# Kernel optimization log

Hardware: AMD Instinct MI355X
Metric: run time of the kernel (lower is better)

Reference implementation:

```python
import jax, jax.numpy as jnp
import numpy as np
import math

IN_C = 1024
OUT_C = 1024
HEADS = 16
GROUPS = 4

def grouped_linear(src, weight, bias):
    # src: [..., in_c]; weight: [g, in_c//g, out_c//g]; bias: [out_c]
    g, icg, ocg = weight.shape
    lead = src.shape[:-1]
    s = src.reshape(*lead, g, icg)
    out = jnp.einsum('...gi,gio->...go', s, weight)
    out = out.reshape(*lead, g * ocg)
    return out + bias

def restricted_softmax(src, margin=0.0):
    src_max = jnp.maximum(jnp.max(src, axis=-1, keepdims=True), 0.0)
    out = jnp.exp(src - src_max)
    return out / (jnp.sum(out, axis=-1, keepdims=True) + jnp.exp(margin - src_max))

def setup_inputs() -> dict:
    key = jax.random.key(0)
    ks = jax.random.split(key, 9)
    B, S = 2, 2048
    icg, ocg = IN_C // GROUPS, OUT_C // GROUPS
    scale = 1.0 / math.sqrt(icg)
    return {
        'query': jax.random.normal(ks[0], (B, S, IN_C), jnp.float32),
        'key': jax.random.normal(ks[1], (B, S, IN_C), jnp.float32),
        'value': jax.random.normal(ks[2], (B, S, IN_C), jnp.float32),
        'wq': jax.random.uniform(ks[3], (GROUPS, icg, ocg), jnp.float32, -scale, scale),
        'wk': jax.random.uniform(ks[4], (GROUPS, icg, ocg), jnp.float32, -scale, scale),
        'wv': jax.random.uniform(ks[5], (GROUPS, icg, ocg), jnp.float32, -scale, scale),
        'bq': jax.random.uniform(ks[6], (OUT_C,), jnp.float32, -scale, scale),
        'bk': jax.random.uniform(ks[7], (OUT_C,), jnp.float32, -scale, scale),
        'bv': jax.random.uniform(ks[8], (OUT_C,), jnp.float32, -scale, scale),
    }

def reference(query, key, value, wq, wk, wv, bq, bk, bv):
    q = grouped_linear(query, wq, bq)   # [B,S,OUT_C]
    k = grouped_linear(key, wk, bk)
    v = grouped_linear(value, wv, bv)
    B, Sq, _ = q.shape
    Sk = k.shape[-2]
    d = OUT_C // HEADS
    q = q.reshape(B, Sq, HEADS, d).transpose(0, 2, 1, 3)  # [B,H,Sq,d]
    k = k.reshape(B, Sk, HEADS, d).transpose(0, 2, 1, 3)
    v = v.reshape(B, Sk, HEADS, d).transpose(0, 2, 1, 3)
    score = jnp.einsum('bhqd,bhkd->bhqk', q, k) / math.sqrt(d)
    attn = restricted_softmax(score)
    out = jnp.einsum('bhqk,bhkd->bhqd', attn, v)
    out = out.transpose(0, 2, 1, 3).reshape(B, Sq, OUT_C)
    return out
```

## Files before the change

kernel.cpp:

```cpp
#include <hip/hip_runtime.h>
#include <hip/hip_bf16.h>

#define BB 2
#define SS 2048
#define CC 1024
#define HH 16
#define DDIM 64
#define NROWS (BB*SS)

#define QSC 0.18033688011112042f

typedef __attribute__((ext_vector_type(8))) short bf16x8;
typedef __attribute__((ext_vector_type(4))) float f32x4;

__device__ __forceinline__ f32x4 mfma16(bf16x8 a, bf16x8 b, f32x4 c) {
    return __builtin_amdgcn_mfma_f32_16x16x32_bf16(a, b, c, 0, 0, 0);
}

__global__ __launch_bounds__(256) void prep_wt(
    const float* __restrict__ wq, const float* __restrict__ wk,
    const float* __restrict__ wv, __hip_bfloat16* __restrict__ wt)
{
    const float* w = blockIdx.z == 0 ? wq : blockIdx.z == 1 ? wk : wv;
    const int g  = blockIdx.y;
    const int kt = blockIdx.x >> 2;
    const int nt = blockIdx.x & 3;
    __shared__ __hip_bfloat16 Ls[64][72];
    const int t = threadIdx.x;
    #pragma unroll
    for (int j = 0; j < 4; ++j) {
        int f4 = t + j*256;
        int row = f4 >> 4, n0 = (f4 & 15) * 4;
        float4 f = *(const float4*)&w[(size_t)g*65536 + (size_t)(kt*64+row)*256
                                      + nt*64 + n0];
        Ls[n0+0][row] = __float2bfloat16(f.x);
        Ls[n0+1][row] = __float2bfloat16(f.y);
        Ls[n0+2][row] = __float2bfloat16(f.z);
        Ls[n0+3][row] = __float2bfloat16(f.w);
    }
    __syncthreads();
    #pragma unroll
    for (int j = 0; j < 2; ++j) {
        int u = t + j*256;
        int nr = u >> 3, k8 = (u & 7) * 8;
        *(uint4*)&wt[((size_t)(blockIdx.z*4 + g)*256 + nt*64 + nr)*256
                     + kt*64 + k8] = *(const uint4*)&Ls[nr][k8];
    }
}

__global__ __launch_bounds__(256, 3) void proj_mfma(
    const float* __restrict__ qin, const float* __restrict__ kin,
    const float* __restrict__ vin,
    const __hip_bfloat16* __restrict__ wt,
    const float* __restrict__ bq, const float* __restrict__ bk,
    const float* __restrict__ bv,
    __hip_bfloat16* __restrict__ qs, __hip_bfloat16* __restrict__ ks_,
    __hip_bfloat16* __restrict__ vs)
{
    const int z = blockIdx.z;
    const float* src; const float* bias;
    if (z == 0)      { src = qin; bias = bq; }
    else if (z == 1) { src = kin; bias = bk; }
    else             { src = vin; bias = bv; }

    const int hp   = blockIdx.y;
    const int g    = hp >> 1;
    const int col0 = (hp & 1) * 128;
    const int row0 = blockIdx.x * 128;
    const int b    = row0 >> 11;
    const int s0   = row0 & 2047;

    __shared__ char smem[36864];
    auto As = (__hip_bfloat16 (*)[72])smem;
    auto Ws = (__hip_bfloat16 (*)[72])(smem + 18432);

    const int t    = threadIdx.x;
    const int wid  = t >> 6;
    const int lane = t & 63;
    const int l16  = lane & 15;
    const int quad = lane >> 4;

    f32x4 acc[2][8];
    #pragma unroll
    for (int mt = 0; mt < 2; ++mt)
        #pragma unroll
        for (int nt = 0; nt < 8; ++nt) acc[mt][nt] = (f32x4){0.f,0.f,0.f,0.f};

    const __hip_bfloat16* wtz = wt + (size_t)(z*4 + g)*65536;

    for (int kt = 0; kt < 4; ++kt) {
        __syncthreads();
        #pragma unroll
        for (int j = 0; j < 8; ++j) {
            int idx = t + j*256;
            int row = idx >> 4, c4 = (idx & 15) * 4;
            float4 f = *(const float4*)&src[(size_t)(row0 + row)*CC + g*256
                                            + kt*64 + c4];
            union { __hip_bfloat16 hh[4]; uint2 u; } pk;
            pk.hh[0] = __float2bfloat16(f.x); pk.hh[1] = __float2bfloat16(f.y);
            pk.hh[2] = __float2bfloat16(f.z); pk.hh[3] = __float2bfloat16(f.w);
            *(uint2*)&As[row][c4] = pk.u;
        }
        #pragma unroll
        for (int j = 0; j < 4; ++j) {
            int idx = t + j*256;
            int n = idx >> 3, k8 = (idx & 7) * 8;
            *(uint4*)&Ws[n][k8] =
                *(const uint4*)&wtz[(size_t)(col0 + n)*256 + kt*64 + k8];
        }
        __syncthreads();
        #pragma unroll
        for (int kss = 0; kss < 2; ++kss) {
            bf16x8 af[2], wf[8];
            #pragma unroll
            for (int mt = 0; mt < 2; ++mt)
                af[mt] = *(const bf16x8*)&As[wid*32 + mt*16 + l16][kss*32 + quad*8];
            #pragma unroll
            for (int nt = 0; nt < 8; ++nt)
                wf[nt] = *(const bf16x8*)&Ws[nt*16 + l16][kss*32 + quad*8];
            #pragma unroll
            for (int mt = 0; mt < 2; ++mt)
                #pragma unroll
                for (int nt = 0; nt < 8; ++nt)
                    acc[mt][nt] = mfma16(af[mt], wf[nt], acc[mt][nt]);
        }
    }

    float bval[8];
    #pragma unroll
    for (int nt = 0; nt < 8; ++nt) bval[nt] = bias[g*256 + col0 + nt*16 + l16];

    __syncthreads();

    if (z < 2) {
        const float scale = (z == 0) ? QSC : 1.0f;
        auto Ot = (__hip_bfloat16 (*)[136])smem;
        #pragma unroll
        for (int mt = 0; mt < 2; ++mt)
            #pragma unroll
            for (int nt = 0; nt < 8; ++nt)
                #pragma unroll
                for (int r = 0; r < 4; ++r)
                    Ot[wid*32 + mt*16 + quad*4 + r][nt*16 + l16] =
                        __float2bfloat16((acc[mt][nt][r] + bval[nt]) * scale);
        __syncthreads();
        __hip_bfloat16* base = (z == 0) ? qs : ks_;
        #pragma unroll
        for (int j = 0; j < 8; ++j) {
            int f = wid + j*4;
            int hl = f >> 4, t16l = (f >> 1) & 7, kcs = f & 1;
            uint4 v = *(const uint4*)&Ot[t16l*16 + l16][hl*64 + kcs*32 + quad*8];
            int h = hp*2 + hl;
            int t16g = (s0 >> 4) + t16l;
            *(uint4*)&base[((size_t)(b*HH + h) << 17)
                           + ((size_t)(t16g*2 + kcs) << 9) + lane*8] = v;
        }
    } else {
        auto Vl = (__hip_bfloat16 (*)[136])smem;
        #pragma unroll
        for (int mt = 0; mt < 2; ++mt)
            #pragma unroll
            for (int nt = 0; nt < 8; ++nt) {
                union { __hip_bfloat16 hh[4]; uint2 u; } pk;
                #pragma unroll
                for (int r = 0; r < 4; ++r)
                    pk.hh[r] = __float2bfloat16(acc[mt][nt][r] + bval[nt]);
                *(uint2*)&Vl[nt*16 + l16][wid*32 + mt*16 + quad*4] = pk.u;
            }
        __syncthreads();
        const int kc0 = s0 >> 5;
        #pragma unroll
        for (int j = 0; j < 8; ++j) {
            int f = wid + j*4;
            int hl = f >> 4, dt = (f >> 2) & 3, kcl = f & 3;
            uint4 v = *(const uint4*)&Vl[hl*64 + dt*16 + l16][kcl*32 + quad*8];
            int h = hp*2 + hl;
            *(uint4*)&vs[((size_t)(b*HH + h) << 17)
                         + ((size_t)(dt*64 + kc0 + kcl) << 9) + lane*8] = v;
        }
    }
}

__global__ __launch_bounds__(256, 2) void attn_mfma(
    const __hip_bfloat16* __restrict__ qs, const __hip_bfloat16* __restrict__ ks_,
    const __hip_bfloat16* __restrict__ vs, float* __restrict__ out)
{
    const int qt = blockIdx.x;
    const int h  = blockIdx.y;
    const int b  = blockIdx.z;

    __shared__ __hip_bfloat16 Ps[4][32][72];

    const int t    = threadIdx.x;
    const int wid  = t >> 6;
    const int lane = t & 63;
    const int l16  = lane & 15;
    const int quad = lane >> 4;

    const __hip_bfloat16* qb = qs + ((size_t)(b*HH + h) << 17);
    const __hip_bfloat16* kb = ks_ + ((size_t)(b*HH + h) << 17);
    const __hip_bfloat16* vb = vs + ((size_t)(b*HH + h) << 17);

    const bf16x8 onesv = (bf16x8){16256,16256,16256,16256,
                                  16256,16256,16256,16256};

    bf16x8 qf[2][2];
    #pragma unroll
    for (int mt = 0; mt < 2; ++mt)
        #pragma unroll
        for (int kss = 0; kss < 2; ++kss)
            qf[mt][kss] = *(const bf16x8*)(qb +
                ((size_t)((qt*8 + wid*2 + mt)*2 + kss) << 9) + lane*8);

    f32x4 O[2][4];
    f32x4 Lfrag[2];
    #pragma unroll
    for (int mt = 0; mt < 2; ++mt) {
        Lfrag[mt] = (f32x4){0.f,0.f,0.f,0.f};
        #pragma unroll
        for (int dt = 0; dt < 4; ++dt) O[mt][dt] = (f32x4){0.f,0.f,0.f,0.f};
    }

    bf16x8 kf[4][2];
    #pragma unroll
    for (int nt = 0; nt < 4; ++nt)
        #pragma unroll
        for (int kss = 0; kss < 2; ++kss)
            kf[nt][kss] = *(const bf16x8*)(kb +
                ((size_t)(nt*2 + kss) << 9) + lane*8);

    for (int kt = 0; kt < SS/64; ++kt) {
        bf16x8 vf[4][2];
        #pragma unroll
        for (int dt = 0; dt < 4; ++dt)
            #pragma unroll
            for (int kss = 0; kss < 2; ++kss)
                vf[dt][kss] = *(const bf16x8*)(vb +
                    ((size_t)(dt*64 + kt*2 + kss) << 9) + lane*8);

        f32x4 st[4][2];
        #pragma unroll
        for (int nt = 0; nt < 4; ++nt)
            #pragma unroll
            for (int mt = 0; mt < 2; ++mt) {
                f32x4 z = (f32x4){0.f,0.f,0.f,0.f};
                z = mfma16(kf[nt][0], qf[mt][0], z);
                st[nt][mt] = mfma16(kf[nt][1], qf[mt][1], z);
            }

        if (kt + 1 < SS/64) {
            #pragma unroll
            for (int nt = 0; nt < 4; ++nt)
                #pragma unroll
                for (int kss = 0; kss < 2; ++kss)
                    kf[nt][kss] = *(const bf16x8*)(kb +
                        ((size_t)((kt+1)*8 + nt*2 + kss) << 9) + lane*8);
        }

        #pragma unroll
        for (int nt = 0; nt < 2; ++nt)
            #pragma unroll
            for (int mt = 0; mt < 2; ++mt) {
                float2 e0, e1;
                e0.x = __builtin_amdgcn_exp2f(st[nt][mt][0]);
                e0.y = __builtin_amdgcn_exp2f(st[nt][mt][1]);
                e1.x = __builtin_amdgcn_exp2f(st[nt][mt][2]);
                e1.y = __builtin_amdgcn_exp2f(st[nt][mt][3]);
                union { __hip_bfloat162 h2[2]; uint2 u; } pk;
                pk.h2[0] = __float22bfloat162_rn(e0);
                pk.h2[1] = __float22bfloat162_rn(e1);
                *(uint2*)&Ps[wid][mt*16 + l16][nt*16 + quad*4] = pk.u;
            }
        bf16x8 pf0[2];
        #pragma unroll
        for (int mt = 0; mt < 2; ++mt)
            pf0[mt] = *(const bf16x8*)&Ps[wid][mt*16 + l16][quad*8];

        #pragma unroll
        for (int nt = 2; nt < 4; ++nt)
            #pragma unroll
            for (int mt = 0; mt < 2; ++mt) {
                float2 e0, e1;
                e0.x = __builtin_amdgcn_exp2f(st[nt][mt][0]);
                e0.y = __builtin_amdgcn_exp2f(st[nt][mt][1]);
                e1.x = __builtin_amdgcn_exp2f(st[nt][mt][2]);
                e1.y = __builtin_amdgcn_exp2f(st[nt][mt][3]);
                union { __hip_bfloat162 h2[2]; uint2 u; } pk;
                pk.h2[0] = __float22bfloat162_rn(e0);
                pk.h2[1] = __float22bfloat162_rn(e1);
                *(uint2*)&Ps[wid][mt*16 + l16][nt*16 + quad*4] = pk.u;
            }
        bf16x8 pf1[2];
        #pragma unroll
        for (int mt = 0; mt < 2; ++mt)
            pf1[mt] = *(const bf16x8*)&Ps[wid][mt*16 + l16][32 + quad*8];

        #pragma unroll
        for (int mt = 0; mt < 2; ++mt) {
            Lfrag[mt] = mfma16(onesv, pf0[mt], Lfrag[mt]);
            #pragma unroll
            for (int dt = 0; dt < 4; ++dt)
                O[mt][dt] = mfma16(vf[dt][0], pf0[mt], O[mt][dt]);
        }
        #pragma unroll
        for (int mt = 0; mt < 2; ++mt) {
            Lfrag[mt] = mfma16(onesv, pf1[mt], Lfrag[mt]);
            #pragma unroll
            for (int dt = 0; dt < 4; ++dt)
                O[mt][dt] = mfma16(vf[dt][1], pf1[mt], O[mt][dt]);
        }
    }

    const int qrow0 = qt*128 + wid*32;
    #pragma unroll
    for (int mt = 0; mt < 2; ++mt) {
        const float inv = 1.0f / (1.0f + Lfrag[mt][0]);
        const size_t row = (size_t)b*SS + qrow0 + mt*16 + l16;
        #pragma unroll
        for (int dt = 0; dt < 4; ++dt) {
            float4 o4;
            o4.x = O[mt][dt][0] * inv;
            o4.y = O[mt][dt][1] * inv;
            o4.z = O[mt][dt][2] * inv;
            o4.w = O[mt][dt][3] * inv;
            *(float4*)&out[row*CC + h*DDIM + dt*16 + quad*4] = o4;
        }
    }
}

extern "C" void kernel_launch(void* const* d_in, const int* in_sizes, int n_in,
                              void* d_out, int out_size, void* d_ws, size_t ws_size,
                              hipStream_t stream) {
    (void)in_sizes; (void)n_in; (void)out_size; (void)ws_size;
    const float* qin = (const float*)d_in[0];
    const float* kin = (const float*)d_in[1];
    const float* vin = (const float*)d_in[2];
    const float* wq  = (const float*)d_in[3];
    const float* wk  = (const float*)d_in[4];
    const float* wv  = (const float*)d_in[5];
    const float* bq  = (const float*)d_in[6];
    const float* bk  = (const float*)d_in[7];
    const float* bv  = (const float*)d_in[8];

    char* w0 = (char*)d_ws;
    __hip_bfloat16* qs = (__hip_bfloat16*)(w0);
    __hip_bfloat16* ks = (__hip_bfloat16*)(w0 + 8388608);
    __hip_bfloat16* vs = (__hip_bfloat16*)(w0 + 16777216);
    __hip_bfloat16* wt = (__hip_bfloat16*)(w0 + 25165824);
    float* out = (float*)d_out;

    prep_wt<<<dim3(16, 4, 3), 256, 0, stream>>>(wq, wk, wv, wt);
    proj_mfma<<<dim3(32, 8, 3), 256, 0, stream>>>(
        qin, kin, vin, wt, bq, bk, bv, qs, ks, vs);
    attn_mfma<<<dim3(16, 16, 2), 256, 0, stream>>>(qs, ks, vs, out);
}
```

Measured before the change: 166.5 us.

## Split key range across wave pairs with larger per-wave query tiles

Each wave now handles 64 query rows instead of 32, and the four waves split into two query halves times two key halves. Partial O and row sums from the second key half are combined through shared memory after a block barrier. This doubles reuse of each loaded K/V fragment across query tiles, cutting global K/V fragment loads per MFMA. The cost is more accumulator registers (O grows to 16 f32x4), which may hurt occupancy at the 2-blocks launch bound, plus a larger LDS footprint and a reduction step.

```diff
diff --git a/kernel.cpp b/kernel.cpp
--- a/kernel.cpp
+++ b/kernel.cpp
@@ -189,10 +189,14 @@
     const int h  = blockIdx.y;
     const int b  = blockIdx.z;
 
-    __shared__ __hip_bfloat16 Ps[4][32][72];
+    __shared__ __hip_bfloat16 Ps[4][64][72];
+    __shared__ float Uls[2][64][68];
+    __shared__ float Lls[2][64];
 
     const int t    = threadIdx.x;
     const int wid  = t >> 6;
+    const int qsub = wid & 1;
+    const int kh   = wid >> 1;
     const int lane = t & 63;
     const int l16  = lane & 15;
     const int quad = lane >> 4;
@@ -204,18 +208,18 @@
     const bf16x8 onesv = (bf16x8){16256,16256,16256,16256,
                                   16256,16256,16256,16256};
 
-    bf16x8 qf[2][2];
-    #pragma unroll
-    for (int mt = 0; mt < 2; ++mt)
+    bf16x8 qf[4][2];
+    #pragma unroll
+    for (int mt = 0; mt < 4; ++mt)
         #pragma unroll
         for (int kss = 0; kss < 2; ++kss)
             qf[mt][kss] = *(const bf16x8*)(qb +
-                ((size_t)((qt*8 + wid*2 + mt)*2 + kss) << 9) + lane*8);
-
-    f32x4 O[2][4];
-    f32x4 Lfrag[2];
-    #pragma unroll
-    for (int mt = 0; mt < 2; ++mt) {
+                ((size_t)((qt*8 + qsub*4 + mt)*2 + kss) << 9) + lane*8);
+
+    f32x4 O[4][4];
+    f32x4 Lfrag[4];
+    #pragma unroll
+    for (int mt = 0; mt < 4; ++mt) {
         Lfrag[mt] = (f32x4){0.f,0.f,0.f,0.f};
         #pragma unroll
         for (int dt = 0; dt < 4; ++dt) O[mt][dt] = (f32x4){0.f,0.f,0.f,0.f};
@@ -227,103 +231,95 @@
         #pragma unroll
         for (int kss = 0; kss < 2; ++kss)
             kf[nt][kss] = *(const bf16x8*)(kb +
-                ((size_t)(nt*2 + kss) << 9) + lane*8);
-
-    for (int kt = 0; kt < SS/64; ++kt) {
+                ((size_t)((kh*64 + nt)*2 + kss) << 9) + lane*8);
+
+    for (int kt = 0; kt < 16; ++kt) {
         bf16x8 vf[4][2];
         #pragma unroll
         for (int dt = 0; dt < 4; ++dt)
             #pragma unroll
             for (int kss = 0; kss < 2; ++kss)
                 vf[dt][kss] = *(const bf16x8*)(vb +
-                    ((size_t)(dt*64 + kt*2 + kss) << 9) + lane*8);
-
-        f32x4 st[4][2];
-        #pragma unroll
-        for (int nt = 0; nt < 4; ++nt)
-            #pragma unroll
-            for (int mt = 0; mt < 2; ++mt) {
+                    ((size_t)(dt*64 + kh*32 + kt*2 + kss) << 9) + lane*8);
+
+        #pragma unroll
+        for (int nt = 0; nt < 4; ++nt) {
+            f32x4 st[4];
+            #pragma unroll
+            for (int mt = 0; mt < 4; ++mt) {
                 f32x4 z = (f32x4){0.f,0.f,0.f,0.f};
                 z = mfma16(kf[nt][0], qf[mt][0], z);
-                st[nt][mt] = mfma16(kf[nt][1], qf[mt][1], z);
-            }
-
-        if (kt + 1 < SS/64) {
-            #pragma unroll
-            for (int nt = 0; nt < 4; ++nt)
-                #pragma unroll
-                for (int kss = 0; kss < 2; ++kss)
-                    kf[nt][kss] = *(const bf16x8*)(kb +
-                        ((size_t)((kt+1)*8 + nt*2 + kss) << 9) + lane*8);
-        }
-
-        #pragma unroll
-        for (int nt = 0; nt < 2; ++nt)
-            #pragma unroll
-            for (int mt = 0; mt < 2; ++mt) {
+                st[mt] = mfma16(kf[nt][1], qf[mt][1], z);
+            }
+            #pragma unroll
+            for (int mt = 0; mt < 4; ++mt) {
                 float2 e0, e1;
-                e0.x = __builtin_amdgcn_exp2f(st[nt][mt][0]);
-                e0.y = __builtin_amdgcn_exp2f(st[nt][mt][1]);
-                e1.x = __builtin_amdgcn_exp2f(st[nt][mt][2]);
-                e1.y = __builtin_amdgcn_exp2f(st[nt][mt][3]);
+                e0.x = __builtin_amdgcn_exp2f(st[mt][0]);
+                e0.y = __builtin_amdgcn_exp2f(st[mt][1]);
+                e1.x = __builtin_amdgcn_exp2f(st[mt][2]);
+                e1.y = __builtin_amdgcn_exp2f(st[mt][3]);
                 union { __hip_bfloat162 h2[2]; uint2 u; } pk;
                 pk.h2[0] = __float22bfloat162_rn(e0);
                 pk.h2[1] = __float22bfloat162_rn(e1);
                 *(uint2*)&Ps[wid][mt*16 + l16][nt*16 + quad*4] = pk.u;
             }
-        bf16x8 pf0[2];
-        #pragma unroll
-        for (int mt = 0; mt < 2; ++mt)
-            pf0[mt] = *(const bf16x8*)&Ps[wid][mt*16 + l16][quad*8];
-
-        #pragma unroll
-        for (int nt = 2; nt < 4; ++nt)
-            #pragma unroll
-            for (int mt = 0; mt < 2; ++mt) {
-                float2 e0, e1;
-                e0.x = __builtin_amdgcn_exp2f(st[nt][mt][0]);
-                e0.y = __builtin_amdgcn_exp2f(st[nt][mt][1]);
-                e1.x = __builtin_amdgcn_exp2f(st[nt][mt][2]);
-                e1.y = __builtin_amdgcn_exp2f(st[nt][mt][3]);
-                union { __hip_bfloat162 h2[2]; uint2 u; } pk;
-                pk.h2[0] = __float22bfloat162_rn(e0);
-                pk.h2[1] = __float22bfloat162_rn(e1);
-                *(uint2*)&Ps[wid][mt*16 + l16][nt*16 + quad*4] = pk.u;
-            }
-        bf16x8 pf1[2];
-        #pragma unroll
-        for (int mt = 0; mt < 2; ++mt)
-            pf1[mt] = *(const bf16x8*)&Ps[wid][mt*16 + l16][32 + quad*8];
-
-        #pragma unroll
-        for (int mt = 0; mt < 2; ++mt) {
-            Lfrag[mt] = mfma16(onesv, pf0[mt], Lfrag[mt]);
-            #pragma unroll
-            for (int dt = 0; dt < 4; ++dt)
-                O[mt][dt] = mfma16(vf[dt][0], pf0[mt], O[mt][dt]);
-        }
-        #pragma unroll
-        for (int mt = 0; mt < 2; ++mt) {
-            Lfrag[mt] = mfma16(onesv, pf1[mt], Lfrag[mt]);
-            #pragma unroll
-            for (int dt = 0; dt < 4; ++dt)
-                O[mt][dt] = mfma16(vf[dt][1], pf1[mt], O[mt][dt]);
-        }
-    }
-
-    const int qrow0 = qt*128 + wid*32;
-    #pragma unroll
-    for (int mt = 0; mt < 2; ++mt) {
-        const float inv = 1.0f / (1.0f + Lfrag[mt][0]);
-        const size_t row = (size_t)b*SS + qrow0 + mt*16 + l16;
-        #pragma unroll
-        for (int dt = 0; dt < 4; ++dt) {
-            float4 o4;
-            o4.x = O[mt][dt][0] * inv;
-            o4.y = O[mt][dt][1] * inv;
-            o4.z = O[mt][dt][2] * inv;
-            o4.w = O[mt][dt][3] * inv;
-            *(float4*)&out[row*CC + h*DDIM + dt*16 + quad*4] = o4;
+        }
+
+        if (kt + 1 < 16) {
+            #pragma unroll
+            for (int nt = 0; nt < 4; ++nt)
+                #pragma unroll
+                for (int kss = 0; kss < 2; ++kss)
+                    kf[nt][kss] = *(const bf16x8*)(kb +
+                        ((size_t)((kh*64 + (kt+1)*4 + nt)*2 + kss) << 9) + lane*8);
+        }
+
+        #pragma unroll
+        for (int kss = 0; kss < 2; ++kss) {
+            bf16x8 pf[4];
+            #pragma unroll
+            for (int mt = 0; mt < 4; ++mt)
+                pf[mt] = *(const bf16x8*)&Ps[wid][mt*16 + l16][kss*32 + quad*8];
+            #pragma unroll
+            for (int mt = 0; mt < 4; ++mt) {
+                Lfrag[mt] = mfma16(onesv, pf[mt], Lfrag[mt]);
+                #pragma unroll
+                for (int dt = 0; dt < 4; ++dt)
+                    O[mt][dt] = mfma16(vf[dt][kss], pf[mt], O[mt][dt]);
+            }
+        }
+    }
+
+    if (kh == 1) {
+        #pragma unroll
+        for (int mt = 0; mt < 4; ++mt) {
+            if (quad == 0) Lls[qsub][mt*16 + l16] = Lfrag[mt][0];
+            #pragma unroll
+            for (int dt = 0; dt < 4; ++dt) {
+                float4 u4;
+                u4.x = O[mt][dt][0]; u4.y = O[mt][dt][1];
+                u4.z = O[mt][dt][2]; u4.w = O[mt][dt][3];
+                *(float4*)&Uls[qsub][mt*16 + l16][dt*16 + quad*4] = u4;
+            }
+        }
+    }
+    __syncthreads();
+    if (kh == 0) {
+        #pragma unroll
+        for (int mt = 0; mt < 4; ++mt) {
+            const float inv = 1.0f /
+                (1.0f + Lfrag[mt][0] + Lls[qsub][mt*16 + l16]);
+            const size_t row = (size_t)b*SS + qt*128 + qsub*64 + mt*16 + l16;
+            #pragma unroll
+            for (int dt = 0; dt < 4; ++dt) {
+                float4 u4 = *(const float4*)&Uls[qsub][mt*16 + l16][dt*16 + quad*4];
+                float4 o4;
+                o4.x = (O[mt][dt][0] + u4.x) * inv;
+                o4.y = (O[mt][dt][1] + u4.y) * inv;
+                o4.z = (O[mt][dt][2] + u4.z) * inv;
+                o4.w = (O[mt][dt][3] + u4.w) * inv;
+                *(float4*)&out[row*CC + h*DDIM + dt*16 + quad*4] = o4;
+            }
         }
     }
 }
```

After: 161.9 us. 1.03x faster.
